# Optimization experiments

Measured on AMD Instinct MI355X. Metric: run time of the kernel, lower is better.

Reference implementation:

```python
import jax, jax.numpy as jnp
import numpy as np

NEG_INF = -1e9  # additive mask value for masked softmax


def setup_inputs() -> dict:
    key = jax.random.key(0)
    k1, k2, k3, k4, k5 = jax.random.split(key, 5)
    bz, rv_num, rv_len, in_feat, out_feat = 32, 10, 128, 300, 128
    seq_a = jax.random.normal(k1, (bz, rv_num, rv_len, in_feat), dtype=jnp.float32)
    seq_b = jax.random.normal(k2, (bz, rv_num, rv_len, in_feat), dtype=jnp.float32)
    mask_a = jax.random.randint(k3, (bz, rv_num, rv_len), 0, 2, dtype=jnp.int32)
    mask_b = jax.random.randint(k4, (bz, rv_num, rv_len), 0, 2, dtype=jnp.int32)
    # guarantee at least one valid position per review (avoid fully-masked rows)
    mask_a = mask_a.at[:, :, 0].set(1)
    mask_b = mask_b.at[:, :, 0].set(1)
    # FC transform params (xavier-normal-ish weight, zero bias)
    W = jax.random.normal(k5, (in_feat, out_feat), dtype=jnp.float32) * (2.0 / np.sqrt(in_feat + out_feat))
    b = jnp.zeros((out_feat,), dtype=jnp.float32)
    return {"seq_a": seq_a, "seq_b": seq_b, "mask_a": mask_a, "mask_b": mask_b, "W": W, "b": b}


def _masked_softmax(scores, mask):
    # scores: [N, L], mask: [N, L] in {0,1}
    logits = jnp.where(mask > 0, scores, NEG_INF)
    return jax.nn.softmax(logits, axis=-1)


def reference(seq_a, seq_b, mask_a, mask_b, W, b):
    bz, rv_num, rv_len, _ = seq_a.shape
    hdim = W.shape[1]
    N = bz * rv_num          # flattened batch of reviews
    M = rv_num * rv_len      # all tokens on the other side

    # FC + ReLU feature transform
    ta = jax.nn.relu(jnp.einsum('bnld,dh->bnlh', seq_a, W) + b)
    tb = jax.nn.relu(jnp.einsum('bnld,dh->bnlh', seq_b, W) + b)

    sa = ta.reshape(N, rv_len, hdim)
    sb = tb.reshape(N, rv_len, hdim)
    # expand: each review attends over ALL tokens of the other sequence in its sample
    ea = jnp.broadcast_to(ta.reshape(bz, 1, M, hdim), (bz, rv_num, M, hdim)).reshape(N, M, hdim)
    eb = jnp.broadcast_to(tb.reshape(bz, 1, M, hdim), (bz, rv_num, M, hdim)).reshape(N, M, hdim)

    # DOT interaction (no scale): affinity [N, rv_len, M]
    atob_aff = jnp.einsum('nld,nmd->nlm', sa, eb)
    btoa_aff = jnp.einsum('nld,nmd->nlm', sb, ea)

    # MEAN pooling over the other-sequence axis
    atob_scores = atob_aff.mean(axis=-1)  # [N, rv_len]
    btoa_scores = btoa_aff.mean(axis=-1)

    ma = mask_a.reshape(N, rv_len)
    mb = mask_b.reshape(N, rv_len)
    atob_w = _masked_softmax(atob_scores, ma)
    btoa_w = _masked_softmax(btoa_scores, mb)

    a_out = jnp.einsum('nl,nld->nd', atob_w, sa)
    b_out = jnp.einsum('nl,nld->nd', btoa_w, sb)
    return (a_out, b_out, atob_w, btoa_w)
```

## Files before the change

kernel.cpp:

```cpp
#include <hip/hip_runtime.h>
#include <hip/hip_bf16.h>


#define K_FEAT 300
#define H 128
#define NTOK 40960
#define NREV 320
#define TOK_PER_SAMPLE 1280
#define BLKS_PER_SAMPLE 10
#define NCHUNK 10
#define WFRAG_ELEMS (NCHUNK * 8 * 2 * 64 * 8)

typedef __attribute__((ext_vector_type(8))) short bf16x8;
typedef __attribute__((ext_vector_type(4))) float f32x4;
typedef unsigned short u16;
typedef unsigned int u32;

static __device__ __forceinline__ u16 f2bf(float x) {
    u32 u = __float_as_uint(x);
    return (u16)((u + 0x7fffu + ((u >> 16) & 1u)) >> 16);
}
static __device__ __forceinline__ float bf2f(u16 s) {
    return __uint_as_float(((u32)s) << 16);
}

union bfpack { uint4 u; bf16x8 v; };

__global__ void wsplit_kernel(const float* __restrict__ W, u16* __restrict__ Wfrag)
{
    int i = blockIdx.x * 256 + threadIdx.x;
    if (i >= WFRAG_ELEMS) return;
    int j    = i & 7;
    int lane = (i >> 3) & 63;
    int part = (i >> 9) & 1;
    int n    = (i >> 10) & 7;
    int c    = i >> 13;
    int h = n * 16 + (lane & 15);
    int k = c * 32 + (lane >> 4) * 8 + j;
    float w = (k < K_FEAT) ? W[(size_t)k * H + h] : 0.f;
    u16 hi = f2bf(w);
    Wfrag[i] = part ? f2bf(w - bf2f(hi)) : hi;
}

__global__ __launch_bounds__(256, 3) void fc_mfma_kernel(
    const float* __restrict__ seq_a, const float* __restrict__ seq_b,
    const u16* __restrict__ Wfrag, const float* __restrict__ bias,
    u16* __restrict__ ta, u16* __restrict__ tb,
    float* __restrict__ psum_a, float* __restrict__ psum_b)
{
    __shared__ float psum_s[4][H];
    __shared__ float bias_s[H];

    int blk = blockIdx.x;
    const float* seq; u16* outp; float* psum;
    if (blk < 320) { seq = seq_a; outp = ta; psum = psum_a; }
    else           { seq = seq_b; outp = tb; psum = psum_b; blk -= 320; }

    const int tid = threadIdx.x;
    const int tok0 = blk * 128;
    const int wave = tid >> 6;
    const int lane = tid & 63;
    const int nn = lane & 15;
    const int quad = lane >> 4;

    if (tid < H) bias_s[tid] = bias[tid];

    const float* row0 = seq + (size_t)(tok0 + wave * 32 + nn) * K_FEAT;
    const float* row1 = row0 + (size_t)16 * K_FEAT;

    f32x4 acc[2][8];
#pragma unroll
    for (int mi = 0; mi < 2; ++mi)
#pragma unroll
        for (int n = 0; n < 8; ++n) acc[mi][n] = (f32x4){0.f, 0.f, 0.f, 0.f};

    float4 pf[2][2];
    {
        int kk = quad * 8;
        pf[0][0] = *(const float4*)&row0[kk];
        pf[0][1] = *(const float4*)&row0[kk + 4];
        pf[1][0] = *(const float4*)&row1[kk];
        pf[1][1] = *(const float4*)&row1[kk + 4];
    }

    for (int c = 0; c < NCHUNK; ++c) {
        bf16x8 ah[2], al[2];
#pragma unroll
        for (int mi = 0; mi < 2; ++mi) {
            float v[8] = {pf[mi][0].x, pf[mi][0].y, pf[mi][0].z, pf[mi][0].w,
                          pf[mi][1].x, pf[mi][1].y, pf[mi][1].z, pf[mi][1].w};
            u16 hh[8];
            bfpack ph, pl;
#pragma unroll
            for (int j = 0; j < 8; ++j) hh[j] = f2bf(v[j]);
            ph.u.x = (u32)hh[0] | ((u32)hh[1] << 16);
            ph.u.y = (u32)hh[2] | ((u32)hh[3] << 16);
            ph.u.z = (u32)hh[4] | ((u32)hh[5] << 16);
            ph.u.w = (u32)hh[6] | ((u32)hh[7] << 16);
            pl.u.x = (u32)f2bf(v[0] - bf2f(hh[0])) | ((u32)f2bf(v[1] - bf2f(hh[1])) << 16);
            pl.u.y = (u32)f2bf(v[2] - bf2f(hh[2])) | ((u32)f2bf(v[3] - bf2f(hh[3])) << 16);
            pl.u.z = (u32)f2bf(v[4] - bf2f(hh[4])) | ((u32)f2bf(v[5] - bf2f(hh[5])) << 16);
            pl.u.w = (u32)f2bf(v[6] - bf2f(hh[6])) | ((u32)f2bf(v[7] - bf2f(hh[7])) << 16);
            ah[mi] = ph.v;
            al[mi] = pl.v;
        }
        if (c < NCHUNK - 1) {
            int kk = (c + 1) * 32 + quad * 8;
            float4 z = make_float4(0.f, 0.f, 0.f, 0.f);
            pf[0][0] = (kk + 4 <= K_FEAT) ? *(const float4*)&row0[kk] : z;
            pf[0][1] = (kk + 8 <= K_FEAT) ? *(const float4*)&row0[kk + 4] : z;
            pf[1][0] = (kk + 4 <= K_FEAT) ? *(const float4*)&row1[kk] : z;
            pf[1][1] = (kk + 8 <= K_FEAT) ? *(const float4*)&row1[kk + 4] : z;
        }
        const u16* wbase = Wfrag + (size_t)c * (8 * 2 * 512);
        bf16x8 wh = *(const bf16x8*)&wbase[0 * 1024 + 0 + lane * 8];
        bf16x8 wl = *(const bf16x8*)&wbase[0 * 1024 + 512 + lane * 8];
#pragma unroll
        for (int n = 0; n < 8; ++n) {
            bf16x8 whc = wh, wlc = wl;
            if (n < 7) {
                wh = *(const bf16x8*)&wbase[(n + 1) * 1024 + 0 + lane * 8];
                wl = *(const bf16x8*)&wbase[(n + 1) * 1024 + 512 + lane * 8];
            }
            acc[0][n] = __builtin_amdgcn_mfma_f32_16x16x32_bf16(whc, ah[0], acc[0][n], 0, 0, 0);
            acc[0][n] = __builtin_amdgcn_mfma_f32_16x16x32_bf16(wlc, ah[0], acc[0][n], 0, 0, 0);
            acc[0][n] = __builtin_amdgcn_mfma_f32_16x16x32_bf16(whc, al[0], acc[0][n], 0, 0, 0);
            acc[1][n] = __builtin_amdgcn_mfma_f32_16x16x32_bf16(whc, ah[1], acc[1][n], 0, 0, 0);
            acc[1][n] = __builtin_amdgcn_mfma_f32_16x16x32_bf16(wlc, ah[1], acc[1][n], 0, 0, 0);
            acc[1][n] = __builtin_amdgcn_mfma_f32_16x16x32_bf16(whc, al[1], acc[1][n], 0, 0, 0);
        }
    }

#pragma unroll
    for (int n = 0; n < 8; ++n) {
        float4 bb = *(const float4*)&bias_s[n * 16 + quad * 4];
#pragma unroll
        for (int mi = 0; mi < 2; ++mi) {
            int tok = tok0 + (wave * 2 + mi) * 16 + nn;
            float v0 = fmaxf(acc[mi][n][0] + bb.x, 0.f);
            float v1 = fmaxf(acc[mi][n][1] + bb.y, 0.f);
            float v2 = fmaxf(acc[mi][n][2] + bb.z, 0.f);
            float v3 = fmaxf(acc[mi][n][3] + bb.w, 0.f);
            acc[mi][n][0] = v0; acc[mi][n][1] = v1;
            acc[mi][n][2] = v2; acc[mi][n][3] = v3;
            uint2 p;
            p.x = (u32)f2bf(v0) | ((u32)f2bf(v1) << 16);
            p.y = (u32)f2bf(v2) | ((u32)f2bf(v3) << 16);
            *(uint2*)&outp[(size_t)tok * H + n * 16 + quad * 4] = p;
        }
    }

#pragma unroll
    for (int n = 0; n < 8; ++n) {
        float s0 = acc[0][n][0] + acc[1][n][0];
        float s1 = acc[0][n][1] + acc[1][n][1];
        float s2 = acc[0][n][2] + acc[1][n][2];
        float s3 = acc[0][n][3] + acc[1][n][3];
        s0 += __shfl_xor(s0, 1); s0 += __shfl_xor(s0, 2); s0 += __shfl_xor(s0, 4); s0 += __shfl_xor(s0, 8);
        s1 += __shfl_xor(s1, 1); s1 += __shfl_xor(s1, 2); s1 += __shfl_xor(s1, 4); s1 += __shfl_xor(s1, 8);
        s2 += __shfl_xor(s2, 1); s2 += __shfl_xor(s2, 2); s2 += __shfl_xor(s2, 4); s2 += __shfl_xor(s2, 8);
        s3 += __shfl_xor(s3, 1); s3 += __shfl_xor(s3, 2); s3 += __shfl_xor(s3, 4); s3 += __shfl_xor(s3, 8);
        if (nn == 0) {
            psum_s[wave][n * 16 + quad * 4 + 0] = s0;
            psum_s[wave][n * 16 + quad * 4 + 1] = s1;
            psum_s[wave][n * 16 + quad * 4 + 2] = s2;
            psum_s[wave][n * 16 + quad * 4 + 3] = s3;
        }
    }
    __syncthreads();
    if (tid < H)
        psum[(size_t)blk * H + tid] = psum_s[0][tid] + psum_s[1][tid]
                                    + psum_s[2][tid] + psum_s[3][tid];
}

__global__ __launch_bounds__(256) void attn_kernel(
    const u16* __restrict__ ta, const u16* __restrict__ tb,
    const int* __restrict__ mask_a, const int* __restrict__ mask_b,
    const float* __restrict__ psum_a, const float* __restrict__ psum_b,
    float* __restrict__ out)
{
    int n = blockIdx.x;
    int side = 0;
    if (n >= NREV) { side = 1; n -= NREV; }

    const u16* t = side ? tb : ta;
    const int* mask = side ? mask_b : mask_a;
    const float* psum_o = side ? psum_a : psum_b;
    float* out_vec = out + (side ? NREV * H : 0);
    float* out_w = out + 2 * NREV * H + (side ? NREV * H : 0);

    int sample = n / 10;
    int tid = threadIdx.x;

    __shared__ float score_part[128 * 17];
    __shared__ float mean_s[128];
    __shared__ float w_s[128];
    __shared__ float red[4];
    __shared__ float part_out[16 * 128];

    if (tid < 128) {
        float s = 0.f;
        const float* pb = psum_o + (size_t)sample * BLKS_PER_SAMPLE * H + tid;
#pragma unroll
        for (int i = 0; i < BLKS_PER_SAMPLE; ++i) s += pb[(size_t)i * H];
        mean_s[tid] = s * (1.0f / (float)TOK_PER_SAMPLE);
    }
    __syncthreads();

    const u16* rowbase = t + (size_t)n * 128 * H;

#pragma unroll
    for (int i = 0; i < 8; ++i) {
        int q = tid + 256 * i;
        int r = q >> 4;
        int c8 = q & 15;
        uint4 v = *(const uint4*)&rowbase[r * H + c8 * 8];
        const float* m = &mean_s[c8 * 8];
        float p = 0.f;
        p += bf2f((u16)(v.x & 0xffff)) * m[0];
        p += bf2f((u16)(v.x >> 16)) * m[1];
        p += bf2f((u16)(v.y & 0xffff)) * m[2];
        p += bf2f((u16)(v.y >> 16)) * m[3];
        p += bf2f((u16)(v.z & 0xffff)) * m[4];
        p += bf2f((u16)(v.z >> 16)) * m[5];
        p += bf2f((u16)(v.w & 0xffff)) * m[6];
        p += bf2f((u16)(v.w >> 16)) * m[7];
        score_part[r * 17 + c8] = p;
    }
    __syncthreads();

    float logit = -1e9f;
    if (tid < 128) {
        float s = 0.f;
#pragma unroll
        for (int j = 0; j < 16; ++j) s += score_part[tid * 17 + j];
        int mv = mask[n * 128 + tid];
        logit = (mv > 0) ? s : -1e9f;
    }

    float mx = logit;
    for (int off = 32; off > 0; off >>= 1) mx = fmaxf(mx, __shfl_xor(mx, off));
    if ((tid & 63) == 0) red[tid >> 6] = mx;
    __syncthreads();
    mx = fmaxf(fmaxf(red[0], red[1]), fmaxf(red[2], red[3]));
    __syncthreads();

    float e = __expf(logit - mx);
    float ssum = e;
    for (int off = 32; off > 0; off >>= 1) ssum += __shfl_xor(ssum, off);
    if ((tid & 63) == 0) red[tid >> 6] = ssum;
    __syncthreads();
    ssum = red[0] + red[1] + red[2] + red[3];

    float w = e / ssum;
    if (tid < 128) {
        w_s[tid] = w;
        out_w[n * 128 + tid] = w;
    }
    __syncthreads();

    int c8 = tid & 15;
    int lp = tid >> 4;
    float o[8] = {0.f, 0.f, 0.f, 0.f, 0.f, 0.f, 0.f, 0.f};
#pragma unroll
    for (int k = 0; k < 8; ++k) {
        int l = k * 16 + lp;
        float wl = w_s[l];
        uint4 v = *(const uint4*)&rowbase[l * H + c8 * 8];
        o[0] = fmaf(wl, bf2f((u16)(v.x & 0xffff)), o[0]);
        o[1] = fmaf(wl, bf2f((u16)(v.x >> 16)), o[1]);
        o[2] = fmaf(wl, bf2f((u16)(v.y & 0xffff)), o[2]);
        o[3] = fmaf(wl, bf2f((u16)(v.y >> 16)), o[3]);
        o[4] = fmaf(wl, bf2f((u16)(v.z & 0xffff)), o[4]);
        o[5] = fmaf(wl, bf2f((u16)(v.z >> 16)), o[5]);
        o[6] = fmaf(wl, bf2f((u16)(v.w & 0xffff)), o[6]);
        o[7] = fmaf(wl, bf2f((u16)(v.w >> 16)), o[7]);
    }
    *(float4*)&part_out[lp * 128 + c8 * 8] = make_float4(o[0], o[1], o[2], o[3]);
    *(float4*)&part_out[lp * 128 + c8 * 8 + 4] = make_float4(o[4], o[5], o[6], o[7]);
    __syncthreads();
    if (tid < 128) {
        float s = 0.f;
#pragma unroll
        for (int p = 0; p < 16; ++p) s += part_out[p * 128 + tid];
        out_vec[n * 128 + tid] = s;
    }
}

extern "C" void kernel_launch(void* const* d_in, const int* in_sizes, int n_in,
                              void* d_out, int out_size, void* d_ws, size_t ws_size,
                              hipStream_t stream)
{
    const float* seq_a = (const float*)d_in[0];
    const float* seq_b = (const float*)d_in[1];
    const int* mask_a = (const int*)d_in[2];
    const int* mask_b = (const int*)d_in[3];
    const float* W = (const float*)d_in[4];
    const float* bias = (const float*)d_in[5];
    float* out = (float*)d_out;

    u16* ta = (u16*)d_ws;
    u16* tb = ta + (size_t)NTOK * H;
    float* psum_a = (float*)(tb + (size_t)NTOK * H);
    float* psum_b = psum_a + NREV * H;
    u16* Wfrag = (u16*)(psum_b + NREV * H);

    wsplit_kernel<<<(WFRAG_ELEMS + 255) / 256, 256, 0, stream>>>(W, Wfrag);
    fc_mfma_kernel<<<640, 256, 0, stream>>>(seq_a, seq_b, Wfrag, bias, ta, tb, psum_a, psum_b);
    attn_kernel<<<640, 256, 0, stream>>>(ta, tb, mask_a, mask_b, psum_a, psum_b, out);
}
```

Before: 173.8 us.

## Stage split-bf16 activation tiles in LDS with coalesced loads and halve tile size

The FC kernel now loads 64-token tiles through coalesced float4 loads by token/column threads. It converts them to hi/lo bf16 once per element and stores them in double-buffered LDS, from which the MFMA fragments are read. The old per-lane strided row loads are replaced, and the grid doubles to 1280 blocks with higher occupancy. The cost is one barrier per K-chunk and LDS traffic. The attention kernel's per-sample block count constant is changed to match the doubled partial sums.

```diff
diff --git a/kernel.cpp b/kernel.cpp
--- a/kernel.cpp
+++ b/kernel.cpp
@@ -7,7 +7,9 @@
 #define NTOK 40960
 #define NREV 320
 #define TOK_PER_SAMPLE 1280
-#define BLKS_PER_SAMPLE 10
+#define BLKS_PER_SAMPLE 20
+#define TM 64
+#define LDA 40
 #define NCHUNK 10
 #define WFRAG_ELEMS (NCHUNK * 8 * 2 * 64 * 8)
 
@@ -23,8 +25,6 @@
 static __device__ __forceinline__ float bf2f(u16 s) {
     return __uint_as_float(((u32)s) << 16);
 }
-
-union bfpack { uint4 u; bf16x8 v; };
 
 __global__ void wsplit_kernel(const float* __restrict__ W, u16* __restrict__ Wfrag)
 {
@@ -42,22 +42,24 @@
     Wfrag[i] = part ? f2bf(w - bf2f(hi)) : hi;
 }
 
-__global__ __launch_bounds__(256, 3) void fc_mfma_kernel(
+__global__ __launch_bounds__(256, 4) void fc_mfma_kernel(
     const float* __restrict__ seq_a, const float* __restrict__ seq_b,
     const u16* __restrict__ Wfrag, const float* __restrict__ bias,
     u16* __restrict__ ta, u16* __restrict__ tb,
     float* __restrict__ psum_a, float* __restrict__ psum_b)
 {
+    __shared__ u16 Ah_s[2][TM * LDA];
+    __shared__ u16 Al_s[2][TM * LDA];
     __shared__ float psum_s[4][H];
     __shared__ float bias_s[H];
 
     int blk = blockIdx.x;
     const float* seq; u16* outp; float* psum;
-    if (blk < 320) { seq = seq_a; outp = ta; psum = psum_a; }
-    else           { seq = seq_b; outp = tb; psum = psum_b; blk -= 320; }
+    if (blk < 640) { seq = seq_a; outp = ta; psum = psum_a; }
+    else           { seq = seq_b; outp = tb; psum = psum_b; blk -= 640; }
 
     const int tid = threadIdx.x;
-    const int tok0 = blk * 128;
+    const int tok0 = blk * TM;
     const int wave = tid >> 6;
     const int lane = tid & 63;
     const int nn = lane & 15;
@@ -65,53 +67,43 @@
 
     if (tid < H) bias_s[tid] = bias[tid];
 
-    const float* row0 = seq + (size_t)(tok0 + wave * 32 + nn) * K_FEAT;
-    const float* row1 = row0 + (size_t)16 * K_FEAT;
-
-    f32x4 acc[2][8];
-#pragma unroll
-    for (int mi = 0; mi < 2; ++mi)
-#pragma unroll
-        for (int n = 0; n < 8; ++n) acc[mi][n] = (f32x4){0.f, 0.f, 0.f, 0.f};
-
-    float4 pf[2][2];
-    {
-        int kk = quad * 8;
-        pf[0][0] = *(const float4*)&row0[kk];
-        pf[0][1] = *(const float4*)&row0[kk + 4];
-        pf[1][0] = *(const float4*)&row1[kk];
-        pf[1][1] = *(const float4*)&row1[kk + 4];
+    const int st_tok = tid >> 3;
+    const int st_j = tid & 7;
+
+    f32x4 acc[8];
+#pragma unroll
+    for (int n = 0; n < 8; ++n) acc[n] = (f32x4){0.f, 0.f, 0.f, 0.f};
+
+    float4 pf[2];
+#pragma unroll
+    for (int it = 0; it < 2; ++it)
+        pf[it] = *(const float4*)&seq[(size_t)(tok0 + st_tok + it * 32) * K_FEAT + 4 * st_j];
+#pragma unroll
+    for (int it = 0; it < 2; ++it) {
+        int t = st_tok + it * 32;
+        float4 v = pf[it];
+        u16 h0 = f2bf(v.x), h1 = f2bf(v.y), h2 = f2bf(v.z), h3 = f2bf(v.w);
+        uint2 hp, lp;
+        hp.x = (u32)h0 | ((u32)h1 << 16);
+        hp.y = (u32)h2 | ((u32)h3 << 16);
+        lp.x = (u32)f2bf(v.x - bf2f(h0)) | ((u32)f2bf(v.y - bf2f(h1)) << 16);
+        lp.y = (u32)f2bf(v.z - bf2f(h2)) | ((u32)f2bf(v.w - bf2f(h3)) << 16);
+        *(uint2*)&Ah_s[0][t * LDA + 4 * st_j] = hp;
+        *(uint2*)&Al_s[0][t * LDA + 4 * st_j] = lp;
     }
 
     for (int c = 0; c < NCHUNK; ++c) {
-        bf16x8 ah[2], al[2];
-#pragma unroll
-        for (int mi = 0; mi < 2; ++mi) {
-            float v[8] = {pf[mi][0].x, pf[mi][0].y, pf[mi][0].z, pf[mi][0].w,
-                          pf[mi][1].x, pf[mi][1].y, pf[mi][1].z, pf[mi][1].w};
-            u16 hh[8];
-            bfpack ph, pl;
-#pragma unroll
-            for (int j = 0; j < 8; ++j) hh[j] = f2bf(v[j]);
-            ph.u.x = (u32)hh[0] | ((u32)hh[1] << 16);
-            ph.u.y = (u32)hh[2] | ((u32)hh[3] << 16);
-            ph.u.z = (u32)hh[4] | ((u32)hh[5] << 16);
-            ph.u.w = (u32)hh[6] | ((u32)hh[7] << 16);
-            pl.u.x = (u32)f2bf(v[0] - bf2f(hh[0])) | ((u32)f2bf(v[1] - bf2f(hh[1])) << 16);
-            pl.u.y = (u32)f2bf(v[2] - bf2f(hh[2])) | ((u32)f2bf(v[3] - bf2f(hh[3])) << 16);
-            pl.u.z = (u32)f2bf(v[4] - bf2f(hh[4])) | ((u32)f2bf(v[5] - bf2f(hh[5])) << 16);
-            pl.u.w = (u32)f2bf(v[6] - bf2f(hh[6])) | ((u32)f2bf(v[7] - bf2f(hh[7])) << 16);
-            ah[mi] = ph.v;
-            al[mi] = pl.v;
+        __syncthreads();
+        if (c < NCHUNK - 1) {
+            int kk = (c + 1) * 32 + 4 * st_j;
+            float4 z = make_float4(0.f, 0.f, 0.f, 0.f);
+#pragma unroll
+            for (int it = 0; it < 2; ++it)
+                pf[it] = (kk + 4 <= K_FEAT)
+                    ? *(const float4*)&seq[(size_t)(tok0 + st_tok + it * 32) * K_FEAT + kk] : z;
         }
-        if (c < NCHUNK - 1) {
-            int kk = (c + 1) * 32 + quad * 8;
-            float4 z = make_float4(0.f, 0.f, 0.f, 0.f);
-            pf[0][0] = (kk + 4 <= K_FEAT) ? *(const float4*)&row0[kk] : z;
-            pf[0][1] = (kk + 8 <= K_FEAT) ? *(const float4*)&row0[kk + 4] : z;
-            pf[1][0] = (kk + 4 <= K_FEAT) ? *(const float4*)&row1[kk] : z;
-            pf[1][1] = (kk + 8 <= K_FEAT) ? *(const float4*)&row1[kk + 4] : z;
-        }
+        bf16x8 ah = *(const bf16x8*)&Ah_s[c & 1][(wave * 16 + nn) * LDA + quad * 8];
+        bf16x8 al = *(const bf16x8*)&Al_s[c & 1][(wave * 16 + nn) * LDA + quad * 8];
         const u16* wbase = Wfrag + (size_t)c * (8 * 2 * 512);
         bf16x8 wh = *(const bf16x8*)&wbase[0 * 1024 + 0 + lane * 8];
         bf16x8 wl = *(const bf16x8*)&wbase[0 * 1024 + 512 + lane * 8];
@@ -122,40 +114,45 @@
                 wh = *(const bf16x8*)&wbase[(n + 1) * 1024 + 0 + lane * 8];
                 wl = *(const bf16x8*)&wbase[(n + 1) * 1024 + 512 + lane * 8];
             }
-            acc[0][n] = __builtin_amdgcn_mfma_f32_16x16x32_bf16(whc, ah[0], acc[0][n], 0, 0, 0);
-            acc[0][n] = __builtin_amdgcn_mfma_f32_16x16x32_bf16(wlc, ah[0], acc[0][n], 0, 0, 0);
-            acc[0][n] = __builtin_amdgcn_mfma_f32_16x16x32_bf16(whc, al[0], acc[0][n], 0, 0, 0);
-            acc[1][n] = __builtin_amdgcn_mfma_f32_16x16x32_bf16(whc, ah[1], acc[1][n], 0, 0, 0);
-            acc[1][n] = __builtin_amdgcn_mfma_f32_16x16x32_bf16(wlc, ah[1], acc[1][n], 0, 0, 0);
-            acc[1][n] = __builtin_amdgcn_mfma_f32_16x16x32_bf16(whc, al[1], acc[1][n], 0, 0, 0);
+            acc[n] = __builtin_amdgcn_mfma_f32_16x16x32_bf16(whc, ah, acc[n], 0, 0, 0);
+            acc[n] = __builtin_amdgcn_mfma_f32_16x16x32_bf16(wlc, ah, acc[n], 0, 0, 0);
+            acc[n] = __builtin_amdgcn_mfma_f32_16x16x32_bf16(whc, al, acc[n], 0, 0, 0);
         }
-    }
-
+        if (c < NCHUNK - 1) {
+#pragma unroll
+            for (int it = 0; it < 2; ++it) {
+                int t = st_tok + it * 32;
+                float4 v = pf[it];
+                u16 h0 = f2bf(v.x), h1 = f2bf(v.y), h2 = f2bf(v.z), h3 = f2bf(v.w);
+                uint2 hp, lp;
+                hp.x = (u32)h0 | ((u32)h1 << 16);
+                hp.y = (u32)h2 | ((u32)h3 << 16);
+                lp.x = (u32)f2bf(v.x - bf2f(h0)) | ((u32)f2bf(v.y - bf2f(h1)) << 16);
+                lp.y = (u32)f2bf(v.z - bf2f(h2)) | ((u32)f2bf(v.w - bf2f(h3)) << 16);
+                *(uint2*)&Ah_s[(c + 1) & 1][t * LDA + 4 * st_j] = hp;
+                *(uint2*)&Al_s[(c + 1) & 1][t * LDA + 4 * st_j] = lp;
+            }
+        }
+    }
+
+    int tok = tok0 + wave * 16 + nn;
 #pragma unroll
     for (int n = 0; n < 8; ++n) {
         float4 bb = *(const float4*)&bias_s[n * 16 + quad * 4];
-#pragma unroll
-        for (int mi = 0; mi < 2; ++mi) {
-            int tok = tok0 + (wave * 2 + mi) * 16 + nn;
-            float v0 = fmaxf(acc[mi][n][0] + bb.x, 0.f);
-            float v1 = fmaxf(acc[mi][n][1] + bb.y, 0.f);
-            float v2 = fmaxf(acc[mi][n][2] + bb.z, 0.f);
-            float v3 = fmaxf(acc[mi][n][3] + bb.w, 0.f);
-            acc[mi][n][0] = v0; acc[mi][n][1] = v1;
-            acc[mi][n][2] = v2; acc[mi][n][3] = v3;
-            uint2 p;
-            p.x = (u32)f2bf(v0) | ((u32)f2bf(v1) << 16);
-            p.y = (u32)f2bf(v2) | ((u32)f2bf(v3) << 16);
-            *(uint2*)&outp[(size_t)tok * H + n * 16 + quad * 4] = p;
-        }
+        float v0 = fmaxf(acc[n][0] + bb.x, 0.f);
+        float v1 = fmaxf(acc[n][1] + bb.y, 0.f);
+        float v2 = fmaxf(acc[n][2] + bb.z, 0.f);
+        float v3 = fmaxf(acc[n][3] + bb.w, 0.f);
+        acc[n][0] = v0; acc[n][1] = v1; acc[n][2] = v2; acc[n][3] = v3;
+        uint2 p;
+        p.x = (u32)f2bf(v0) | ((u32)f2bf(v1) << 16);
+        p.y = (u32)f2bf(v2) | ((u32)f2bf(v3) << 16);
+        *(uint2*)&outp[(size_t)tok * H + n * 16 + quad * 4] = p;
     }
 
 #pragma unroll
     for (int n = 0; n < 8; ++n) {
-        float s0 = acc[0][n][0] + acc[1][n][0];
-        float s1 = acc[0][n][1] + acc[1][n][1];
-        float s2 = acc[0][n][2] + acc[1][n][2];
-        float s3 = acc[0][n][3] + acc[1][n][3];
+        float s0 = acc[n][0], s1 = acc[n][1], s2 = acc[n][2], s3 = acc[n][3];
         s0 += __shfl_xor(s0, 1); s0 += __shfl_xor(s0, 2); s0 += __shfl_xor(s0, 4); s0 += __shfl_xor(s0, 8);
         s1 += __shfl_xor(s1, 1); s1 += __shfl_xor(s1, 2); s1 += __shfl_xor(s1, 4); s1 += __shfl_xor(s1, 8);
         s2 += __shfl_xor(s2, 1); s2 += __shfl_xor(s2, 2); s2 += __shfl_xor(s2, 4); s2 += __shfl_xor(s2, 8);
@@ -302,10 +299,10 @@
     u16* ta = (u16*)d_ws;
     u16* tb = ta + (size_t)NTOK * H;
     float* psum_a = (float*)(tb + (size_t)NTOK * H);
-    float* psum_b = psum_a + NREV * H;
-    u16* Wfrag = (u16*)(psum_b + NREV * H);
+    float* psum_b = psum_a + 640 * H;
+    u16* Wfrag = (u16*)(psum_b + 640 * H);
 
     wsplit_kernel<<<(WFRAG_ELEMS + 255) / 256, 256, 0, stream>>>(W, Wfrag);
-    fc_mfma_kernel<<<640, 256, 0, stream>>>(seq_a, seq_b, Wfrag, bias, ta, tb, psum_a, psum_b);
+    fc_mfma_kernel<<<1280, 256, 0, stream>>>(seq_a, seq_b, Wfrag, bias, ta, tb, psum_a, psum_b);
     attn_kernel<<<640, 256, 0, stream>>>(ta, tb, mask_a, mask_b, psum_a, psum_b, out);
 }
```

Result: slower. 189.2 us (+8.8%).
